# Kernel tuning notes

Measured on AMD Instinct MI355X. Metric: run time of the kernel, lower is better.

## Reference

```python
import jax, jax.numpy as jnp
import numpy as np
from functools import partial

V, E, H, F = 32000, 256, 512, 256  # vocab, embed_dim, hidden_dim, num_filters
FS = (3, 4, 5)

def setup_inputs() -> dict:
    key = jax.random.key(0)
    ks = jax.random.split(key, 24)
    s = 0.02
    d = {}
    d["src"] = jax.random.randint(ks[0], (32, 512), 0, V)
    d["trg"] = jax.random.randint(ks[1], (32, 64), 0, V)
    # embeddings with padding_idx=0 zeroed
    d["enc_emb"] = (jax.random.normal(ks[2], (V, E)) * s).at[0].set(0.0)
    d["dec_emb"] = (jax.random.normal(ks[3], (V, E)) * s).at[0].set(0.0)
    # conv1d weights (out_channels=F, in_channels=E, kernel)
    d["conv_w3"] = jax.random.normal(ks[4], (F, E, 3)) * s
    d["conv_b3"] = jnp.zeros((F,))
    d["conv_w4"] = jax.random.normal(ks[5], (F, E, 4)) * s
    d["conv_b4"] = jnp.zeros((F,))
    d["conv_w5"] = jax.random.normal(ks[6], (F, E, 5)) * s
    d["conv_b5"] = jnp.zeros((F,))
    d["fc1_w"] = jax.random.normal(ks[7], (H, 3 * F)) * s
    d["fc1_b"] = jnp.zeros((H,))
    d["fc2_w"] = jax.random.normal(ks[8], (H, H)) * s
    d["fc2_b"] = jnp.zeros((H,))
    # 2-layer LSTM: layer1 input E+H, layer2 input H; gates order i,f,g,o
    d["w_ih1"] = jax.random.normal(ks[9], (4 * H, E + H)) * s
    d["w_hh1"] = jax.random.normal(ks[10], (4 * H, H)) * s
    d["b_ih1"] = jnp.zeros((4 * H,))
    d["b_hh1"] = jnp.zeros((4 * H,))
    d["w_ih2"] = jax.random.normal(ks[11], (4 * H, H)) * s
    d["w_hh2"] = jax.random.normal(ks[12], (4 * H, H)) * s
    d["b_ih2"] = jnp.zeros((4 * H,))
    d["b_hh2"] = jnp.zeros((4 * H,))
    d["out_w"] = jax.random.normal(ks[13], (V, H)) * s
    d["out_b"] = jnp.zeros((V,))
    return d

def _lstm_cell(x, h, c, w_ih, w_hh, b_ih, b_hh):
    gates = x @ w_ih.T + b_ih + h @ w_hh.T + b_hh  # (B, 4H)
    i, f, g, o = jnp.split(gates, 4, axis=-1)
    c_new = jax.nn.sigmoid(f) * c + jax.nn.sigmoid(i) * jnp.tanh(g)
    h_new = jax.nn.sigmoid(o) * jnp.tanh(c_new)
    return h_new, c_new

def _encoder(src, enc_emb, convs, fc1_w, fc1_b, fc2_w, fc2_b):
    x = enc_emb[src]                    # (B, S, E)
    x = jnp.transpose(x, (0, 2, 1))     # (B, E, S)
    pooled = []
    for w, b in convs:
        y = jax.lax.conv_general_dilated(
            x, w, window_strides=(1,), padding='VALID',
            dimension_numbers=('NCH', 'OIH', 'NCH'))  # (B, F, S-k+1)
        pooled.append(jnp.max(jax.nn.relu(y + b[None, :, None]), axis=2))
    cat = jnp.concatenate(pooled, axis=1)              # (B, 3F)
    h = jax.nn.relu(cat @ fc1_w.T + fc1_b)             # (B, H)
    return h @ fc2_w.T + fc2_b                         # (B, H)

def reference(src, trg, enc_emb, conv_w3, conv_b3, conv_w4, conv_b4,
              conv_w5, conv_b5, fc1_w, fc1_b, fc2_w, fc2_b, dec_emb,
              w_ih1, w_hh1, b_ih1, b_hh1, w_ih2, w_hh2, b_ih2, b_hh2,
              out_w, out_b):
    B, T = trg.shape
    enc_out = _encoder(src, enc_emb,
                       [(conv_w3, conv_b3), (conv_w4, conv_b4), (conv_w5, conv_b5)],
                       fc1_w, fc1_b, fc2_w, fc2_b)  # (B, H)

    def step(carry, tok):
        h1, c1, h2, c2 = carry
        x = jnp.concatenate([dec_emb[tok], enc_out], axis=1)  # (B, E+H)
        h1, c1 = _lstm_cell(x, h1, c1, w_ih1, w_hh1, b_ih1, b_hh1)
        h2, c2 = _lstm_cell(h1, h2, c2, w_ih2, w_hh2, b_ih2, b_hh2)
        logits = h2 @ out_w.T + out_b                          # (B, V)
        return (h1, c1, h2, c2), logits

    z = jnp.zeros((B, H), dtype=enc_out.dtype)
    tokens = trg[:, :-1].T  # teacher forcing (ratio=1.0): (T-1, B)
    _, logits = jax.lax.scan(step, (z, z, z, z), tokens)       # (T-1, B, V)
    logits = jnp.transpose(logits, (1, 0, 2))                  # (B, T-1, V)
    # outputs[:, 0] is left as zeros, matching the torch loop starting at t=1
    return jnp.concatenate([jnp.zeros((B, 1, logits.shape[-1]), logits.dtype), logits], axis=1)
```

## Files before the change

kernel.cpp:

```cpp
#include <hip/hip_runtime.h>
#include <math.h>
#include <stdint.h>

#define B_    32
#define E_    256
#define F_    256
#define H_    512
#define V_    32000
#define G4    2048

typedef unsigned short u16;
typedef unsigned long long u64;
typedef __attribute__((ext_vector_type(8))) short bf16x8;
typedef __attribute__((ext_vector_type(4))) float f32x4;

__device__ __forceinline__ float fsig(float x) {
  return __builtin_amdgcn_rcpf(1.f + __expf(-x));
}
__device__ __forceinline__ float ftanh(float x) {
  return 1.f - 2.f * __builtin_amdgcn_rcpf(1.f + __expf(2.f * x));
}

__device__ __forceinline__ u16 f2bf(float f) {
  uint32_t u = __float_as_uint(f);
  uint32_t r = (u + 0x7FFFu + ((u >> 16) & 1u)) >> 16;
  return (u16)r;
}
__device__ __forceinline__ uint32_t pack2(float a, float b) {
  return (uint32_t)f2bf(a) | ((uint32_t)f2bf(b) << 16);
}

#define GLOAD16(gp, lp) __builtin_amdgcn_global_load_lds( \
    (const __attribute__((address_space(1))) uint32_t*)(const void*)(gp), \
    (__attribute__((address_space(3))) uint32_t*)(void*)(lp), 16, 0, 0)

#define ALOAD(P) __hip_atomic_load((P), __ATOMIC_RELAXED, __HIP_MEMORY_SCOPE_AGENT)
#define ASTORE(P, V) __hip_atomic_store((P), (V), __ATOMIC_RELAXED, __HIP_MEMORY_SCOPE_AGENT)

__global__ void prep_all(float* pooled, uint32_t* sent1, uint32_t* sent2,
                         uint32_t* cnt1, u16* h1d, u16* h2a,
                         const float* bi1, const float* bh1,
                         const float* bi2, const float* bh2,
                         float* bs1, float* bs2, float* out,
                         const float* s0, u16* d0, const float* s1, u16* d1,
                         const float* s2, u16* d2, const float* s3, u16* d3,
                         const float* s4, u16* d4,
                         const float* w3, u16* t3, const float* w4, u16* t4,
                         const float* w5, u16* t5) {
  int i = blockIdx.x * blockDim.x + threadIdx.x, st = gridDim.x * blockDim.x;
  for (int k = i; k < 2637824; k += st) {
    int j = k; const float* s; u16* d;
    if (j < 2048000) { s = s0; d = d0; }
    else if ((j -= 2048000) < 196608) { s = s1; d = d1; }
    else if ((j -= 196608) < 131072) { s = s2; d = d2; }
    else if ((j -= 131072) < 131072) { s = s3; d = d3; }
    else { j -= 131072; s = s4; d = d4; }
    const float4* sp = (const float4*)s + 2 * (size_t)j;
    float4 a = sp[0], b = sp[1];
    uint4 u;
    u.x = pack2(a.x, a.y); u.y = pack2(a.z, a.w);
    u.z = pack2(b.x, b.y); u.w = pack2(b.z, b.w);
    *((uint4*)d + j) = u;
  }
  for (int k = i; k < 786432; k += st) {
    int j = k; const float* w; u16* wt; int kw;
    if (j < 196608) { w = w3; wt = t3; kw = 3; }
    else if ((j -= 196608) < 262144) { w = w4; wt = t4; kw = 4; }
    else { j -= 262144; w = w5; wt = t5; kw = 5; }
    int f = j / (kw * 256);
    int r = j - f * (kw * 256);
    int jj = r >> 8, e = r & 255;
    wt[j] = f2bf(w[(f * 256 + e) * kw + jj]);
  }
  for (int k = i; k < 24576; k += st) pooled[k] = 0.f;
  for (int k = i; k < 131072; k += st) {
    uint32_t v = (k < 2048 && (k & 15) == 0) ? 1u : 0u;
    sent1[k] = v; sent2[k] = v;
  }
  for (int k = i; k < 256; k += st) cnt1[k] = 0u;
  uint4 z = {0u, 0u, 0u, 0u};
  for (int k = i; k < 2048; k += st) { ((uint4*)h1d)[k] = z; ((uint4*)h2a)[k] = z; }
  for (int k = i; k < G4; k += st) { bs1[k] = bi1[k] + bh1[k]; bs2[k] = bi2[k] + bh2[k]; }
  for (int k = i; k < B_ * V_; k += st) {
    int b = k / V_, v = k - b * V_;
    __builtin_nontemporal_store(0.f, &out[(size_t)b * 64 * V_ + v]);
  }
}

__global__ void gemm_small(const float* __restrict__ A, const float* __restrict__ W,
                           const float* __restrict__ bias, float* __restrict__ C,
                           int K, int N, int relu) {
  int nl = threadIdx.x & 7, b = threadIdx.x >> 3;
  int n = blockIdx.x * 8 + nl;
  const float* a = A + b * K;
  const float* w = W + (size_t)n * K;
  float acc = 0.f;
  for (int k = 0; k < K; k += 4) {
    float4 av = *reinterpret_cast<const float4*>(&a[k]);
    float4 wv = *reinterpret_cast<const float4*>(&w[k]);
    acc = fmaf(av.x, wv.x, acc); acc = fmaf(av.y, wv.y, acc);
    acc = fmaf(av.z, wv.z, acc); acc = fmaf(av.w, wv.w, acc);
  }
  acc += bias[n];
  if (relu) acc = fmaxf(acc, 0.f);
  C[b * N + n] = acc;
}

__global__ __launch_bounds__(256)
void conv_mfma(const u16* __restrict__ wt3, const u16* __restrict__ wt4,
               const u16* __restrict__ wt5,
               const float* __restrict__ cb3, const float* __restrict__ cb4,
               const float* __restrict__ cb5,
               float* __restrict__ pooled,
               const int* __restrict__ srcTok, const float* __restrict__ emb) {
  const int z = blockIdx.z;
  const u16* Bw = (z == 0) ? wt3 : (z == 1) ? wt4 : wt5;
  const float* bias = (z == 0) ? cb3 : (z == 1) ? cb4 : cb5;
  const int K = 768 + 256 * z, kw = 3 + z, poolOff = 256 * z;

  __shared__ char smem[32768];
  const int tid = threadIdx.x;
  const int wid = tid >> 6, lane = tid & 63;
  const int hi = lane >> 4, lo = lane & 15;
  const int wr = wid >> 1, wc = wid & 1;
  const int m0 = blockIdx.x * 128, n0 = blockIdx.y * 128;
  const int NT = K >> 5;
  const int srow = lane >> 2, sc = lane & 3;

  f32x4 acc[4][4];
#pragma unroll
  for (int i = 0; i < 4; ++i)
#pragma unroll
    for (int j = 0; j < 4; ++j) acc[i][j] = (f32x4){0.f, 0.f, 0.f, 0.f};

  for (int t = -1; t < NT; ++t) {
    int ts = t + 1;
    if (ts < NT) {
      char* base = smem + (ts & 1) * 16384;
      int k0 = ts << 5;
      {
        int j = k0 >> 8, e0 = k0 & 255;
        int row = tid >> 1;
        int m = m0 + row;
        int s = m & 511, b = m >> 9;
        int sj = s + j;
        int tok = (sj < 512) ? srcTok[b * 512 + sj] : -1;
#pragma unroll
        for (int q = 0; q < 2; ++q) {
          int cg = (tid & 1) * 2 + q;
          uint4 u;
          if (tok >= 0) {
            const float* ep = emb + (size_t)tok * 256 + e0 + cg * 8;
            float4 f0 = *(const float4*)(ep);
            float4 f1 = *(const float4*)(ep + 4);
            u.x = pack2(f0.x, f0.y); u.y = pack2(f0.z, f0.w);
            u.z = pack2(f1.x, f1.y); u.w = pack2(f1.z, f1.w);
          } else u = (uint4){0, 0, 0, 0};
          int c = cg ^ (row & 3);
          *(uint4*)(base + row * 64 + c * 16) = u;
        }
      }
#pragma unroll
      for (int q = 0; q < 2; ++q) {
        int row = (wid + q * 4) * 16 + srow;
        int gc = sc ^ (row & 3);
        const char* gp = (const char*)Bw + (((size_t)(n0 + row) * K + k0) << 1) + gc * 16;
        GLOAD16(gp, base + 8192 + (wid + q * 4) * 1024);
      }
    }
    if (t >= 0) {
      char* base = smem + (t & 1) * 16384;
      bf16x8 af[4], bfr[4];
#pragma unroll
      for (int mi = 0; mi < 4; ++mi) {
        int row = wr * 64 + mi * 16 + lo;
        af[mi] = *(const bf16x8*)(base + row * 64 + ((hi ^ (row & 3)) << 4));
      }
#pragma unroll
      for (int ni = 0; ni < 4; ++ni) {
        int row = wc * 64 + ni * 16 + lo;
        bfr[ni] = *(const bf16x8*)(base + 8192 + row * 64 + ((hi ^ (row & 3)) << 4));
      }
#pragma unroll
      for (int mi = 0; mi < 4; ++mi)
#pragma unroll
        for (int ni = 0; ni < 4; ++ni)
          acc[mi][ni] = __builtin_amdgcn_mfma_f32_16x16x32_bf16(af[mi], bfr[ni], acc[mi][ni], 0, 0, 0);
    }
    __syncthreads();
  }

  int b = m0 >> 9;
  int slim = 512 - kw;
#pragma unroll
  for (int ni = 0; ni < 4; ++ni) {
    int col = n0 + wc * 64 + ni * 16 + lo;
    float bv = bias[col];
    float mx = 0.f;
#pragma unroll
    for (int mi = 0; mi < 4; ++mi)
#pragma unroll
      for (int r = 0; r < 4; ++r) {
        int m = m0 + wr * 64 + mi * 16 + hi * 4 + r;
        int s = m & 511;
        float v = acc[mi][ni][r] + bv;
        if (s <= slim && v > mx) mx = v;
      }
    atomicMax((int*)&pooled[b * 768 + poolOff + col], __float_as_int(mx));
  }
}

__global__ __launch_bounds__(256, 1)
void lstm_fused(float* __restrict__ pre,
                const u16* __restrict__ whh1,
                const u16* __restrict__ wih2, const u16* __restrict__ whh2,
                const float* __restrict__ bs2,
                uint32_t* __restrict__ sent1, uint32_t* __restrict__ sent2,
                uint32_t* __restrict__ cnt1,
                u16* __restrict__ h1d, u16* __restrict__ h2a,
                const u16* __restrict__ outw_bf, const float* __restrict__ outb,
                float* __restrict__ out,
                const int* __restrict__ trg, const float* __restrict__ demb,
                const float* __restrict__ enco,
                const u16* __restrict__ wih1_bf, const float* __restrict__ bs1) {
  __shared__ char smem[74752];
  const int tid = threadIdx.x;
  const int wid = tid >> 6, lane = tid & 63, hi = lane >> 4, lo = lane & 15;
  const int hrow = tid >> 3, k8 = tid & 7;
  const int pb = hrow, pj0 = k8 * 2;

#define WAVE_DRAIN() asm volatile("s_waitcnt vmcnt(0)" ::: "memory")
#define POLL1(P) while (ALOAD(P) == 0u) __builtin_amdgcn_s_sleep(1);
#define POLL2(P, Q) for (;;) { uint32_t x_ = ALOAD(P), y_ = ALOAD(Q); \
                               if (x_ & y_) break; __builtin_amdgcn_s_sleep(1); }
#define POLL2S(P, Q) for (;;) { uint32_t x_ = ALOAD(P), y_ = ALOAD(Q); \
                                if (x_ & y_) break; __builtin_amdgcn_s_sleep(16); }

  if (blockIdx.x < 32) {
    const int bi = blockIdx.x;
    u16* hlds = (u16*)smem;
    float* glds = (float*)(smem + 33280);

    bf16x8 wreg[16];
    const u16* wp = whh1 + (((size_t)(wid * 512 + bi * 16 + lo)) << 9) + hi * 8;
#pragma unroll
    for (int ks = 0; ks < 16; ++ks) wreg[ks] = *(const bf16x8*)(wp + ks * 32);

    float creg0 = 0.f, creg1 = 0.f;

    for (int t = 0; t < 63; ++t) {
      if ((t & 3) == 0) {
        if (tid == 0)
          while (ALOAD(cnt1 + (t >> 2) * 16) < 16u) __builtin_amdgcn_s_sleep(8);
        __syncthreads();
      }
      const float* pr = pre + (((size_t)(t * 32 + pb)) << 11) + bi * 16 + pj0;
      float pi0 = pr[0], pf0 = pr[512], pg0 = pr[1024], po0 = pr[1536];
      float pi1 = pr[1], pf1 = pr[513], pg1 = pr[1025], po1 = pr[1537];

      const u64* hp = (const u64*)(h1d + ((size_t)t * 32 + hrow) * 512);
      f32x4 acc0 = (f32x4){0.f,0.f,0.f,0.f}, acc1 = (f32x4){0.f,0.f,0.f,0.f};

      POLL1(sent1 + (size_t)t * 2048 + lane * 16)
      {
        u64 v[8];
#pragma unroll
        for (int g = 0; g < 4; ++g) {
          int c = k8 + 8 * g;
          v[2*g]   = ALOAD(hp + 2 * c);
          v[2*g+1] = ALOAD(hp + 2 * c + 1);
        }
#pragma unroll
        for (int g = 0; g < 4; ++g) {
          int c = k8 + 8 * g;
          u64 w2[2] = { v[2*g], v[2*g+1] };
          *(uint4*)(hlds + hrow * 520 + c * 8) = *(const uint4*)w2;
        }
      }
      __syncthreads();
#pragma unroll
      for (int ks = 0; ks < 8; ++ks) {
        int cg = (ks * 4 + hi) * 8;
        bf16x8 a0 = *(const bf16x8*)(hlds + lo * 520 + cg);
        bf16x8 a1 = *(const bf16x8*)(hlds + (16 + lo) * 520 + cg);
        acc0 = __builtin_amdgcn_mfma_f32_16x16x32_bf16(a0, wreg[ks], acc0, 0, 0, 0);
        acc1 = __builtin_amdgcn_mfma_f32_16x16x32_bf16(a1, wreg[ks], acc1, 0, 0, 0);
      }
      POLL1(sent1 + (size_t)t * 2048 + (64 + lane) * 16)
      {
        u64 v[8];
#pragma unroll
        for (int g = 0; g < 4; ++g) {
          int c = 32 + k8 + 8 * g;
          v[2*g]   = ALOAD(hp + 2 * c);
          v[2*g+1] = ALOAD(hp + 2 * c + 1);
        }
#pragma unroll
        for (int g = 0; g < 4; ++g) {
          int c = 32 + k8 + 8 * g;
          u64 w2[2] = { v[2*g], v[2*g+1] };
          *(uint4*)(hlds + hrow * 520 + c * 8) = *(const uint4*)w2;
        }
      }
      __syncthreads();
#pragma unroll
      for (int ks = 8; ks < 16; ++ks) {
        int cg = (ks * 4 + hi) * 8;
        bf16x8 a0 = *(const bf16x8*)(hlds + lo * 520 + cg);
        bf16x8 a1 = *(const bf16x8*)(hlds + (16 + lo) * 520 + cg);
        acc0 = __builtin_amdgcn_mfma_f32_16x16x32_bf16(a0, wreg[ks], acc0, 0, 0, 0);
        acc1 = __builtin_amdgcn_mfma_f32_16x16x32_bf16(a1, wreg[ks], acc1, 0, 0, 0);
      }
#pragma unroll
      for (int r = 0; r < 4; ++r) {
        glds[wid * 544 + (hi * 4 + r) * 17 + lo] = acc0[r];
        glds[wid * 544 + (16 + hi * 4 + r) * 17 + lo] = acc1[r];
      }
      __syncthreads();

      float iv0 = glds[0*544 + pb*17 + pj0]   + pi0, fv0 = glds[1*544 + pb*17 + pj0]   + pf0;
      float gv0 = glds[2*544 + pb*17 + pj0]   + pg0, ov0 = glds[3*544 + pb*17 + pj0]   + po0;
      float iv1 = glds[0*544 + pb*17 + pj0+1] + pi1, fv1 = glds[1*544 + pb*17 + pj0+1] + pf1;
      float gv1 = glds[2*544 + pb*17 + pj0+1] + pg1, ov1 = glds[3*544 + pb*17 + pj0+1] + po1;
      float cn0 = fsig(fv0) * creg0 + fsig(iv0) * ftanh(gv0);
      float hn0 = fsig(ov0) * ftanh(cn0);
      float cn1 = fsig(fv1) * creg1 + fsig(iv1) * ftanh(gv1);
      float hn1 = fsig(ov1) * ftanh(cn1);
      creg0 = cn0; creg1 = cn1;
      ASTORE((uint32_t*)(h1d + ((size_t)(t + 1) * 32 + pb) * 512 + bi * 16 + pj0),
             pack2(hn0, hn1));
      WAVE_DRAIN();
      if (lane == 0)
        ASTORE(sent1 + (size_t)(t + 1) * 2048 + (bi * 4 + wid) * 16, 1u);
    }
  } else if (blockIdx.x < 64) {
    const int bi2 = blockIdx.x - 32;
    u16* alds = (u16*)smem;
    float* glds = (float*)(smem + 66048);

    bf16x8 wreg[32];
    {
      const u16* wa = wih2 + (((size_t)(wid * 512 + bi2 * 16 + lo)) << 9) + hi * 8;
      const u16* wb = whh2 + (((size_t)(wid * 512 + bi2 * 16 + lo)) << 9) + hi * 8;
#pragma unroll
      for (int ks = 0; ks < 16; ++ks) {
        wreg[ks]      = *(const bf16x8*)(wa + ks * 32);
        wreg[16 + ks] = *(const bf16x8*)(wb + ks * 32);
      }
    }
    float bsv0 = bs2[0 * 512 + bi2 * 16 + pj0], bsv0b = bs2[0 * 512 + bi2 * 16 + pj0 + 1];
    float bsv1 = bs2[1 * 512 + bi2 * 16 + pj0], bsv1b = bs2[1 * 512 + bi2 * 16 + pj0 + 1];
    float bsv2 = bs2[2 * 512 + bi2 * 16 + pj0], bsv2b = bs2[2 * 512 + bi2 * 16 + pj0 + 1];
    float bsv3 = bs2[3 * 512 + bi2 * 16 + pj0], bsv3b = bs2[3 * 512 + bi2 * 16 + pj0 + 1];

    float creg0 = 0.f, creg1 = 0.f;

    for (int t = 0; t < 63; ++t) {
      f32x4 acc0 = (f32x4){0.f,0.f,0.f,0.f}, acc1 = (f32x4){0.f,0.f,0.f,0.f};

      POLL2(sent1 + (size_t)(t + 1) * 2048 + lane * 16,
            sent1 + (size_t)(t + 1) * 2048 + (64 + lane) * 16)
      {
        const u64* hp1 = (const u64*)(h1d + ((size_t)(t + 1) * 32 + hrow) * 512);
        u64 v[16];
#pragma unroll
        for (int g = 0; g < 8; ++g) {
          int c = k8 + 8 * g;
          v[2*g]   = ALOAD(hp1 + 2 * c);
          v[2*g+1] = ALOAD(hp1 + 2 * c + 1);
        }
#pragma unroll
        for (int g = 0; g < 8; ++g) {
          int c = k8 + 8 * g;
          u64 w2[2] = { v[2*g], v[2*g+1] };
          *(uint4*)(alds + hrow * 1032 + c * 8) = *(const uint4*)w2;
        }
      }
      __syncthreads();
#pragma unroll
      for (int ks = 0; ks < 16; ++ks) {
        int cg = (ks * 4 + hi) * 8;
        bf16x8 a0 = *(const bf16x8*)(alds + lo * 1032 + cg);
        bf16x8 a1 = *(const bf16x8*)(alds + (16 + lo) * 1032 + cg);
        acc0 = __builtin_amdgcn_mfma_f32_16x16x32_bf16(a0, wreg[ks], acc0, 0, 0, 0);
        acc1 = __builtin_amdgcn_mfma_f32_16x16x32_bf16(a1, wreg[ks], acc1, 0, 0, 0);
      }
      POLL2(sent2 + (size_t)t * 2048 + lane * 16,
            sent2 + (size_t)t * 2048 + (64 + lane) * 16)
      {
        const u64* hp2 = (const u64*)(h2a + ((size_t)t * 32 + hrow) * 512);
        u64 v[16];
#pragma unroll
        for (int g = 0; g < 8; ++g) {
          int c = k8 + 8 * g;
          v[2*g]   = ALOAD(hp2 + 2 * c);
          v[2*g+1] = ALOAD(hp2 + 2 * c + 1);
        }
#pragma unroll
        for (int g = 0; g < 8; ++g) {
          int c = 64 + k8 + 8 * g;
          u64 w2[2] = { v[2*g], v[2*g+1] };
          *(uint4*)(alds + hrow * 1032 + c * 8) = *(const uint4*)w2;
        }
      }
      __syncthreads();
#pragma unroll
      for (int ks = 0; ks < 16; ++ks) {
        int cg = (64 + ks * 4 + hi) * 8;
        bf16x8 a0 = *(const bf16x8*)(alds + lo * 1032 + cg);
        bf16x8 a1 = *(const bf16x8*)(alds + (16 + lo) * 1032 + cg);
        acc0 = __builtin_amdgcn_mfma_f32_16x16x32_bf16(a0, wreg[16 + ks], acc0, 0, 0, 0);
        acc1 = __builtin_amdgcn_mfma_f32_16x16x32_bf16(a1, wreg[16 + ks], acc1, 0, 0, 0);
      }
#pragma unroll
      for (int r = 0; r < 4; ++r) {
        glds[wid * 544 + (hi * 4 + r) * 17 + lo] = acc0[r];
        glds[wid * 544 + (16 + hi * 4 + r) * 17 + lo] = acc1[r];
      }
      __syncthreads();

      float gi0 = glds[0*544 + pb*17 + pj0]   + bsv0,  gf0 = glds[1*544 + pb*17 + pj0]   + bsv1;
      float gg0 = glds[2*544 + pb*17 + pj0]   + bsv2,  go0 = glds[3*544 + pb*17 + pj0]   + bsv3;
      float gi1 = glds[0*544 + pb*17 + pj0+1] + bsv0b, gf1 = glds[1*544 + pb*17 + pj0+1] + bsv1b;
      float gg1 = glds[2*544 + pb*17 + pj0+1] + bsv2b, go1 = glds[3*544 + pb*17 + pj0+1] + bsv3b;
      float cn0 = fsig(gf0) * creg0 + fsig(gi0) * ftanh(gg0);
      float hn0 = fsig(go0) * ftanh(cn0);
      float cn1 = fsig(gf1) * creg1 + fsig(gi1) * ftanh(gg1);
      float hn1 = fsig(go1) * ftanh(cn1);
      creg0 = cn0; creg1 = cn1;
      ASTORE((uint32_t*)(h2a + ((size_t)(t + 1) * 32 + pb) * 512 + bi2 * 16 + pj0),
             pack2(hn0, hn1));
      WAVE_DRAIN();
      if (lane == 0)
        ASTORE(sent2 + (size_t)(t + 1) * 2048 + (bi2 * 4 + wid) * 16, 1u);
    }
  } else {
    const int bid2 = blockIdx.x - 64;
    const int wr = wid >> 1, wc = wid & 1;
    const int srow = lane >> 2, sc = lane & 3;

    for (int w = bid2; w < 256; w += 160) {
      int rt = w >> 4, ct = w & 15;
      const int m0 = rt * 128, n0 = ct * 128;
      f32x4 acc[4][4];
#pragma unroll
      for (int i = 0; i < 4; ++i)
#pragma unroll
        for (int j = 0; j < 4; ++j) acc[i][j] = (f32x4){0.f, 0.f, 0.f, 0.f};

      for (int t = -1; t < 24; ++t) {
        int ts = t + 1;
        if (ts < 24) {
          char* base = smem + (ts & 1) * 16384;
          int k0 = ts << 5;
          {
            int row = tid >> 1;
            int m = m0 + row;
            int tt = m >> 5, b = m & 31;
            int ok = (m < 2016);
            int tok = ok ? trg[b * 64 + tt] : 0;
#pragma unroll
            for (int q = 0; q < 2; ++q) {
              int cg = (tid & 1) * 2 + q;
              int k = k0 + cg * 8;
              uint4 u;
              if (ok) {
                const float* ep = (k < 256) ? (demb + (size_t)tok * 256 + k)
                                            : (enco + (size_t)b * 512 + (k - 256));
                float4 f0 = *(const float4*)(ep);
                float4 f1 = *(const float4*)(ep + 4);
                u.x = pack2(f0.x, f0.y); u.y = pack2(f0.z, f0.w);
                u.z = pack2(f1.x, f1.y); u.w = pack2(f1.z, f1.w);
              } else u = (uint4){0, 0, 0, 0};
              int c = cg ^ (row & 3);
              *(uint4*)(base + row * 64 + c * 16) = u;
            }
          }
#pragma unroll
          for (int q = 0; q < 2; ++q) {
            int row = (wid + q * 4) * 16 + srow;
            int gc = sc ^ (row & 3);
            const char* gp = (const char*)wih1_bf + (((size_t)(n0 + row) * 768 + k0) << 1) + gc * 16;
            GLOAD16(gp, base + 8192 + (wid + q * 4) * 1024);
          }
        }
        if (t >= 0) {
          char* base = smem + (t & 1) * 16384;
          bf16x8 af[4], bfr[4];
#pragma unroll
          for (int mi = 0; mi < 4; ++mi) {
            int row = wr * 64 + mi * 16 + lo;
            af[mi] = *(const bf16x8*)(base + row * 64 + ((hi ^ (row & 3)) << 4));
          }
#pragma unroll
          for (int ni = 0; ni < 4; ++ni) {
            int row = wc * 64 + ni * 16 + lo;
            bfr[ni] = *(const bf16x8*)(base + 8192 + row * 64 + ((hi ^ (row & 3)) << 4));
          }
#pragma unroll
          for (int mi = 0; mi < 4; ++mi)
#pragma unroll
            for (int ni = 0; ni < 4; ++ni)
              acc[mi][ni] = __builtin_amdgcn_mfma_f32_16x16x32_bf16(af[mi], bfr[ni], acc[mi][ni], 0, 0, 0);
        }
        __syncthreads();
      }
#pragma unroll
      for (int mi = 0; mi < 4; ++mi)
#pragma unroll
        for (int r = 0; r < 4; ++r) {
          int m = m0 + wr * 64 + mi * 16 + hi * 4 + r;
          if (m >= 2016) continue;
#pragma unroll
          for (int ni = 0; ni < 4; ++ni) {
            int col = n0 + wc * 64 + ni * 16 + lo;
            ASTORE((uint32_t*)(pre + (size_t)m * 2048 + col),
                   __float_as_uint(acc[mi][ni][r] + bs1[col]));
          }
        }
      WAVE_DRAIN();
      __syncthreads();
      if (tid == 0)
        __hip_atomic_fetch_add(cnt1 + rt * 16, 1u, __ATOMIC_RELAXED, __HIP_MEMORY_SCOPE_AGENT);
      __syncthreads();
    }

    const u16* A = h2a + 16384;

    for (int ct = bid2; ct < 250; ct += 160) {
      for (int rt = 0; rt < 16; ++rt) {
        int tf = rt * 4 + 4; if (tf > 63) tf = 63;
        if (wid == 0)
          POLL2S(sent2 + (size_t)tf * 2048 + lane * 16,
                 sent2 + (size_t)tf * 2048 + (64 + lane) * 16)
        __syncthreads();

        const int m0 = rt * 128, n0 = ct * 128;
        f32x4 acc[4][4];
#pragma unroll
        for (int i = 0; i < 4; ++i)
#pragma unroll
          for (int j = 0; j < 4; ++j) acc[i][j] = (f32x4){0.f, 0.f, 0.f, 0.f};

        for (int t = -1; t < 16; ++t) {
          int ts = t + 1;
          if (ts < 16) {
            char* base = smem + (ts & 1) * 16384;
            int k0 = ts << 5;
#pragma unroll
            for (int q = 0; q < 2; ++q) {
              int row = (wid + q * 4) * 16 + srow;
              int gc = sc ^ (row & 3);
              const char* gp = (const char*)A + (((size_t)(m0 + row) * 512 + k0) << 1) + gc * 16;
              GLOAD16(gp, base + (wid + q * 4) * 1024);
            }
#pragma unroll
            for (int q = 0; q < 2; ++q) {
              int row = (wid + q * 4) * 16 + srow;
              int gc = sc ^ (row & 3);
              const char* gp = (const char*)outw_bf + (((size_t)(n0 + row) * 512 + k0) << 1) + gc * 16;
              GLOAD16(gp, base + 8192 + (wid + q * 4) * 1024);
            }
          }
          if (t >= 0) {
            char* base = smem + (t & 1) * 16384;
            bf16x8 af[4], bfr[4];
#pragma unroll
            for (int mi = 0; mi < 4; ++mi) {
              int row = wr * 64 + mi * 16 + lo;
              af[mi] = *(const bf16x8*)(base + row * 64 + ((hi ^ (row & 3)) << 4));
            }
#pragma unroll
            for (int ni = 0; ni < 4; ++ni) {
              int row = wc * 64 + ni * 16 + lo;
              bfr[ni] = *(const bf16x8*)(base + 8192 + row * 64 + ((hi ^ (row & 3)) << 4));
            }
#pragma unroll
            for (int mi = 0; mi < 4; ++mi)
#pragma unroll
              for (int ni = 0; ni < 4; ++ni)
                acc[mi][ni] = __builtin_amdgcn_mfma_f32_16x16x32_bf16(af[mi], bfr[ni], acc[mi][ni], 0, 0, 0);
          }
          __syncthreads();
        }

#pragma unroll
        for (int mi = 0; mi < 4; ++mi)
#pragma unroll
          for (int r = 0; r < 4; ++r) {
            int m = m0 + wr * 64 + mi * 16 + hi * 4 + r;
            if (m >= 2016) continue;
            int t2 = m >> 5, b = m & 31;
            size_t rowbase = ((size_t)b * 64 + t2 + 1) * (size_t)V_;
#pragma unroll
            for (int ni = 0; ni < 4; ++ni) {
              int col = n0 + wc * 64 + ni * 16 + lo;
              __builtin_nontemporal_store(acc[mi][ni][r] + outb[col], &out[rowbase + col]);
            }
          }
      }
    }
  }
#undef POLL1
#undef POLL2
#undef POLL2S
#undef WAVE_DRAIN
}

extern "C" void kernel_launch(void* const* d_in, const int* in_sizes, int n_in,
                              void* d_out, int out_size, void* d_ws, size_t ws_size,
                              hipStream_t stream) {
  const int*   src  = (const int*)  d_in[0];
  const int*   trg  = (const int*)  d_in[1];
  const float* eemb = (const float*)d_in[2];
  const float* demb = (const float*)d_in[3];
  const float* cw3  = (const float*)d_in[4];
  const float* cb3  = (const float*)d_in[5];
  const float* cw4  = (const float*)d_in[6];
  const float* cb4  = (const float*)d_in[7];
  const float* cw5  = (const float*)d_in[8];
  const float* cb5  = (const float*)d_in[9];
  const float* fc1w = (const float*)d_in[10];
  const float* fc1b = (const float*)d_in[11];
  const float* fc2w = (const float*)d_in[12];
  const float* fc2b = (const float*)d_in[13];
  const float* wih1 = (const float*)d_in[14];
  const float* whh1 = (const float*)d_in[15];
  const float* bih1 = (const float*)d_in[16];
  const float* bhh1 = (const float*)d_in[17];
  const float* wih2 = (const float*)d_in[18];
  const float* whh2 = (const float*)d_in[19];
  const float* bih2 = (const float*)d_in[20];
  const float* bhh2 = (const float*)d_in[21];
  const float* outw = (const float*)d_in[22];
  const float* outb = (const float*)d_in[23];
  float* out = (float*)d_out;

  uint32_t* sent1 = (uint32_t*)d_ws;
  uint32_t* sent2 = sent1 + 131072;
  uint32_t* cnt1  = sent2 + 131072;
  u16* h1d      = (u16*)(cnt1 + 256);
  u16* h2a      = h1d + 1048576;
  float* pooled = (float*)(h2a + 1048576);
  float* ench   = pooled + 24576;
  float* enco   = ench + 16384;
  float* bs1    = enco + 16384;
  float* bs2    = bs1 + 2048;
  float* pre    = bs2 + 2048;
  u16* outw_bf  = (u16*)(pre + 4128768);
  u16* wih1_bf  = outw_bf + 16384000;
  u16* wih2_bf  = wih1_bf + 1572864;
  u16* whh1_bf  = wih2_bf + 1048576;
  u16* whh2_bf  = whh1_bf + 1048576;
  u16* wtj3     = whh2_bf + 1048576;
  u16* wtj4     = wtj3 + 196608;
  u16* wtj5     = wtj4 + 262144;

  prep_all<<<1024, 256, 0, stream>>>(pooled, sent1, sent2, cnt1, h1d, h2a,
                                     bih1, bhh1, bih2, bhh2, bs1, bs2, out,
                                     outw, outw_bf, wih1, wih1_bf, wih2, wih2_bf,
                                     whh1, whh1_bf, whh2, whh2_bf,
                                     cw3, wtj3, cw4, wtj4, cw5, wtj5);

  conv_mfma<<<dim3(128, 2, 3), 256, 0, stream>>>(wtj3, wtj4, wtj5, cb3, cb4, cb5,
                                                 pooled, src, eemb);
  gemm_small<<<64, 256, 0, stream>>>(pooled, fc1w, fc1b, ench, 768, 512, 1);
  gemm_small<<<64, 256, 0, stream>>>(ench, fc2w, fc2b, enco, 512, 512, 0);

  lstm_fused<<<224, 256, 0, stream>>>(pre, whh1_bf, wih2_bf, whh2_bf, bs2,
                                      sent1, sent2, cnt1, h1d, h2a,
                                      outw_bf, outb, out,
                                      trg, demb, enco, wih1_bf, bs1);
}
```

Baseline: 576.7 us.

## Fuse encoder conv, FC layers and weight casts into persistent LSTM kernel

Moves the conv+maxpool MFMA encoder, both FC layers, and the out_w bf16 conversion into the persistent lstm_fused kernel's worker blocks, coordinated by atomic counters. The LSTM recurrent weights are now converted from fp32 to bf16 directly into registers at kernel start instead of in a separate prep pass. The output GEMM loop is reordered by row-tile batches so earlier time steps can be processed first. This removes several kernel launches and serial dependencies so encoder work and weight casting can overlap with the LSTM recurrence, at the cost of spin-wait synchronisation and more complex inter-block ordering.

After: 635.1 us. 1.1x slower.

```diff
diff --git a/kernel.cpp b/kernel.cpp
--- a/kernel.cpp
+++ b/kernel.cpp
@@ -37,30 +37,22 @@
 #define ALOAD(P) __hip_atomic_load((P), __ATOMIC_RELAXED, __HIP_MEMORY_SCOPE_AGENT)
 #define ASTORE(P, V) __hip_atomic_store((P), (V), __ATOMIC_RELAXED, __HIP_MEMORY_SCOPE_AGENT)
 
-__global__ void prep_all(float* pooled, uint32_t* sent1, uint32_t* sent2,
-                         uint32_t* cnt1, u16* h1d, u16* h2a,
-                         const float* bi1, const float* bh1,
-                         const float* bi2, const float* bh2,
-                         float* bs1, float* bs2, float* out,
-                         const float* s0, u16* d0, const float* s1, u16* d1,
-                         const float* s2, u16* d2, const float* s3, u16* d3,
-                         const float* s4, u16* d4,
-                         const float* w3, u16* t3, const float* w4, u16* t4,
-                         const float* w5, u16* t5) {
+__global__ void prep_small(float* pooled, uint32_t* sent1, uint32_t* sent2,
+                           uint32_t* cnt1, uint32_t* cnts, u16* h1d, u16* h2a,
+                           const float* bi1, const float* bh1,
+                           const float* bi2, const float* bh2,
+                           float* bs1, float* bs2, float* out,
+                           const float* wih1, u16* wih1_bf,
+                           const float* w3, u16* t3, const float* w4, u16* t4,
+                           const float* w5, u16* t5) {
   int i = blockIdx.x * blockDim.x + threadIdx.x, st = gridDim.x * blockDim.x;
-  for (int k = i; k < 2637824; k += st) {
-    int j = k; const float* s; u16* d;
-    if (j < 2048000) { s = s0; d = d0; }
-    else if ((j -= 2048000) < 196608) { s = s1; d = d1; }
-    else if ((j -= 196608) < 131072) { s = s2; d = d2; }
-    else if ((j -= 131072) < 131072) { s = s3; d = d3; }
-    else { j -= 131072; s = s4; d = d4; }
-    const float4* sp = (const float4*)s + 2 * (size_t)j;
+  for (int j = i; j < 196608; j += st) {
+    const float4* sp = (const float4*)wih1 + 2 * (size_t)j;
     float4 a = sp[0], b = sp[1];
     uint4 u;
     u.x = pack2(a.x, a.y); u.y = pack2(a.z, a.w);
     u.z = pack2(b.x, b.y); u.w = pack2(b.z, b.w);
-    *((uint4*)d + j) = u;
+    *((uint4*)wih1_bf + j) = u;
   }
   for (int k = i; k < 786432; k += st) {
     int j = k; const float* w; u16* wt; int kw;
@@ -78,6 +70,7 @@
     sent1[k] = v; sent2[k] = v;
   }
   for (int k = i; k < 256; k += st) cnt1[k] = 0u;
+  for (int k = i; k < 64; k += st) cnts[k] = 0u;
   uint4 z = {0u, 0u, 0u, 0u};
   for (int k = i; k < 2048; k += st) { ((uint4*)h1d)[k] = z; ((uint4*)h2a)[k] = z; }
   for (int k = i; k < G4; k += st) { bs1[k] = bi1[k] + bh1[k]; bs2[k] = bi2[k] + bh2[k]; }
@@ -87,142 +80,27 @@
   }
 }
 
-__global__ void gemm_small(const float* __restrict__ A, const float* __restrict__ W,
-                           const float* __restrict__ bias, float* __restrict__ C,
-                           int K, int N, int relu) {
-  int nl = threadIdx.x & 7, b = threadIdx.x >> 3;
-  int n = blockIdx.x * 8 + nl;
-  const float* a = A + b * K;
-  const float* w = W + (size_t)n * K;
-  float acc = 0.f;
-  for (int k = 0; k < K; k += 4) {
-    float4 av = *reinterpret_cast<const float4*>(&a[k]);
-    float4 wv = *reinterpret_cast<const float4*>(&w[k]);
-    acc = fmaf(av.x, wv.x, acc); acc = fmaf(av.y, wv.y, acc);
-    acc = fmaf(av.z, wv.z, acc); acc = fmaf(av.w, wv.w, acc);
-  }
-  acc += bias[n];
-  if (relu) acc = fmaxf(acc, 0.f);
-  C[b * N + n] = acc;
-}
-
-__global__ __launch_bounds__(256)
-void conv_mfma(const u16* __restrict__ wt3, const u16* __restrict__ wt4,
-               const u16* __restrict__ wt5,
-               const float* __restrict__ cb3, const float* __restrict__ cb4,
-               const float* __restrict__ cb5,
-               float* __restrict__ pooled,
-               const int* __restrict__ srcTok, const float* __restrict__ emb) {
-  const int z = blockIdx.z;
-  const u16* Bw = (z == 0) ? wt3 : (z == 1) ? wt4 : wt5;
-  const float* bias = (z == 0) ? cb3 : (z == 1) ? cb4 : cb5;
-  const int K = 768 + 256 * z, kw = 3 + z, poolOff = 256 * z;
-
-  __shared__ char smem[32768];
-  const int tid = threadIdx.x;
-  const int wid = tid >> 6, lane = tid & 63;
-  const int hi = lane >> 4, lo = lane & 15;
-  const int wr = wid >> 1, wc = wid & 1;
-  const int m0 = blockIdx.x * 128, n0 = blockIdx.y * 128;
-  const int NT = K >> 5;
-  const int srow = lane >> 2, sc = lane & 3;
-
-  f32x4 acc[4][4];
-#pragma unroll
-  for (int i = 0; i < 4; ++i)
-#pragma unroll
-    for (int j = 0; j < 4; ++j) acc[i][j] = (f32x4){0.f, 0.f, 0.f, 0.f};
-
-  for (int t = -1; t < NT; ++t) {
-    int ts = t + 1;
-    if (ts < NT) {
-      char* base = smem + (ts & 1) * 16384;
-      int k0 = ts << 5;
-      {
-        int j = k0 >> 8, e0 = k0 & 255;
-        int row = tid >> 1;
-        int m = m0 + row;
-        int s = m & 511, b = m >> 9;
-        int sj = s + j;
-        int tok = (sj < 512) ? srcTok[b * 512 + sj] : -1;
-#pragma unroll
-        for (int q = 0; q < 2; ++q) {
-          int cg = (tid & 1) * 2 + q;
-          uint4 u;
-          if (tok >= 0) {
-            const float* ep = emb + (size_t)tok * 256 + e0 + cg * 8;
-            float4 f0 = *(const float4*)(ep);
-            float4 f1 = *(const float4*)(ep + 4);
-            u.x = pack2(f0.x, f0.y); u.y = pack2(f0.z, f0.w);
-            u.z = pack2(f1.x, f1.y); u.w = pack2(f1.z, f1.w);
-          } else u = (uint4){0, 0, 0, 0};
-          int c = cg ^ (row & 3);
-          *(uint4*)(base + row * 64 + c * 16) = u;
-        }
-      }
-#pragma unroll
-      for (int q = 0; q < 2; ++q) {
-        int row = (wid + q * 4) * 16 + srow;
-        int gc = sc ^ (row & 3);
-        const char* gp = (const char*)Bw + (((size_t)(n0 + row) * K + k0) << 1) + gc * 16;
-        GLOAD16(gp, base + 8192 + (wid + q * 4) * 1024);
-      }
-    }
-    if (t >= 0) {
-      char* base = smem + (t & 1) * 16384;
-      bf16x8 af[4], bfr[4];
-#pragma unroll
-      for (int mi = 0; mi < 4; ++mi) {
-        int row = wr * 64 + mi * 16 + lo;
-        af[mi] = *(const bf16x8*)(base + row * 64 + ((hi ^ (row & 3)) << 4));
-      }
-#pragma unroll
-      for (int ni = 0; ni < 4; ++ni) {
-        int row = wc * 64 + ni * 16 + lo;
-        bfr[ni] = *(const bf16x8*)(base + 8192 + row * 64 + ((hi ^ (row & 3)) << 4));
-      }
-#pragma unroll
-      for (int mi = 0; mi < 4; ++mi)
-#pragma unroll
-        for (int ni = 0; ni < 4; ++ni)
-          acc[mi][ni] = __builtin_amdgcn_mfma_f32_16x16x32_bf16(af[mi], bfr[ni], acc[mi][ni], 0, 0, 0);
-    }
-    __syncthreads();
-  }
-
-  int b = m0 >> 9;
-  int slim = 512 - kw;
-#pragma unroll
-  for (int ni = 0; ni < 4; ++ni) {
-    int col = n0 + wc * 64 + ni * 16 + lo;
-    float bv = bias[col];
-    float mx = 0.f;
-#pragma unroll
-    for (int mi = 0; mi < 4; ++mi)
-#pragma unroll
-      for (int r = 0; r < 4; ++r) {
-        int m = m0 + wr * 64 + mi * 16 + hi * 4 + r;
-        int s = m & 511;
-        float v = acc[mi][ni][r] + bv;
-        if (s <= slim && v > mx) mx = v;
-      }
-    atomicMax((int*)&pooled[b * 768 + poolOff + col], __float_as_int(mx));
-  }
-}
-
 __global__ __launch_bounds__(256, 1)
 void lstm_fused(float* __restrict__ pre,
-                const u16* __restrict__ whh1,
-                const u16* __restrict__ wih2, const u16* __restrict__ whh2,
+                const float* __restrict__ whh1f,
+                const float* __restrict__ wih2f, const float* __restrict__ whh2f,
                 const float* __restrict__ bs2,
                 uint32_t* __restrict__ sent1, uint32_t* __restrict__ sent2,
-                uint32_t* __restrict__ cnt1,
+                uint32_t* __restrict__ cnt1, uint32_t* __restrict__ cnts,
                 u16* __restrict__ h1d, u16* __restrict__ h2a,
-                const u16* __restrict__ outw_bf, const float* __restrict__ outb,
-                float* __restrict__ out,
+                const float* __restrict__ outwf, u16* __restrict__ outw_bf,
+                const float* __restrict__ outb, float* __restrict__ out,
                 const int* __restrict__ trg, const float* __restrict__ demb,
-                const float* __restrict__ enco,
-                const u16* __restrict__ wih1_bf, const float* __restrict__ bs1) {
+                float* __restrict__ enco,
+                const u16* __restrict__ wih1_bf, const float* __restrict__ bs1,
+                const int* __restrict__ src, const float* __restrict__ eemb,
+                const u16* __restrict__ wtj3, const u16* __restrict__ wtj4,
+                const u16* __restrict__ wtj5,
+                const float* __restrict__ cb3, const float* __restrict__ cb4,
+                const float* __restrict__ cb5,
+                const float* __restrict__ fc1w, const float* __restrict__ fc1b,
+                const float* __restrict__ fc2w, const float* __restrict__ fc2b,
+                float* __restrict__ pooled, float* __restrict__ ench) {
   __shared__ char smem[74752];
   const int tid = threadIdx.x;
   const int wid = tid >> 6, lane = tid & 63, hi = lane >> 4, lo = lane & 15;
@@ -235,6 +113,8 @@
                                if (x_ & y_) break; __builtin_amdgcn_s_sleep(1); }
 #define POLL2S(P, Q) for (;;) { uint32_t x_ = ALOAD(P), y_ = ALOAD(Q); \
                                 if (x_ & y_) break; __builtin_amdgcn_s_sleep(16); }
+#define WAITCNT(P, TGT) { if (tid == 0) while (ALOAD(P) < (uint32_t)(TGT)) \
+                            __builtin_amdgcn_s_sleep(8); __syncthreads(); }
 
   if (blockIdx.x < 32) {
     const int bi = blockIdx.x;
@@ -242,18 +122,23 @@
     float* glds = (float*)(smem + 33280);
 
     bf16x8 wreg[16];
-    const u16* wp = whh1 + (((size_t)(wid * 512 + bi * 16 + lo)) << 9) + hi * 8;
-#pragma unroll
-    for (int ks = 0; ks < 16; ++ks) wreg[ks] = *(const bf16x8*)(wp + ks * 32);
+    {
+      const float* wp = whh1f + (((size_t)(wid * 512 + bi * 16 + lo)) << 9) + hi * 8;
+#pragma unroll
+      for (int ks = 0; ks < 16; ++ks) {
+        float4 f0 = *(const float4*)(wp + ks * 32);
+        float4 f1 = *(const float4*)(wp + ks * 32 + 4);
+        uint4 uu;
+        uu.x = pack2(f0.x, f0.y); uu.y = pack2(f0.z, f0.w);
+        uu.z = pack2(f1.x, f1.y); uu.w = pack2(f1.z, f1.w);
+        wreg[ks] = *(bf16x8*)&uu;
+      }
+    }
 
     float creg0 = 0.f, creg1 = 0.f;
 
     for (int t = 0; t < 63; ++t) {
-      if ((t & 3) == 0) {
-        if (tid == 0)
-          while (ALOAD(cnt1 + (t >> 2) * 16) < 16u) __builtin_amdgcn_s_sleep(8);
-        __syncthreads();
-      }
+      if ((t & 3) == 0) WAITCNT(cnt1 + (t >> 2) * 16, 16)
       const float* pr = pre + (((size_t)(t * 32 + pb)) << 11) + bi * 16 + pj0;
       float pi0 = pr[0], pf0 = pr[512], pg0 = pr[1024], po0 = pr[1536];
       float pi1 = pr[1], pf1 = pr[513], pg1 = pr[1025], po1 = pr[1537];
@@ -340,12 +225,21 @@
 
     bf16x8 wreg[32];
     {
-      const u16* wa = wih2 + (((size_t)(wid * 512 + bi2 * 16 + lo)) << 9) + hi * 8;
-      const u16* wb = whh2 + (((size_t)(wid * 512 + bi2 * 16 + lo)) << 9) + hi * 8;
+      const float* wa = wih2f + (((size_t)(wid * 512 + bi2 * 16 + lo)) << 9) + hi * 8;
+      const float* wb = whh2f + (((size_t)(wid * 512 + bi2 * 16 + lo)) << 9) + hi * 8;
 #pragma unroll
       for (int ks = 0; ks < 16; ++ks) {
-        wreg[ks]      = *(const bf16x8*)(wa + ks * 32);
-        wreg[16 + ks] = *(const bf16x8*)(wb + ks * 32);
+        float4 f0 = *(const float4*)(wa + ks * 32);
+        float4 f1 = *(const float4*)(wa + ks * 32 + 4);
+        uint4 uu;
+        uu.x = pack2(f0.x, f0.y); uu.y = pack2(f0.z, f0.w);
+        uu.z = pack2(f1.x, f1.y); uu.w = pack2(f1.z, f1.w);
+        wreg[ks] = *(bf16x8*)&uu;
+        f0 = *(const float4*)(wb + ks * 32);
+        f1 = *(const float4*)(wb + ks * 32 + 4);
+        uu.x = pack2(f0.x, f0.y); uu.y = pack2(f0.z, f0.w);
+        uu.z = pack2(f1.x, f1.y); uu.w = pack2(f1.z, f1.w);
+        wreg[16 + ks] = *(bf16x8*)&uu;
       }
     }
     float bsv0 = bs2[0 * 512 + bi2 * 16 + pj0], bsv0b = bs2[0 * 512 + bi2 * 16 + pj0 + 1];
@@ -439,6 +333,160 @@
     const int wr = wid >> 1, wc = wid & 1;
     const int srow = lane >> 2, sc = lane & 3;
 
+    for (int w = bid2; w < 768; w += 160) {
+      int z = w >> 8, r2 = w & 255, mt = r2 >> 1, nt = r2 & 1;
+      const u16* Bw = (z == 0) ? wtj3 : (z == 1) ? wtj4 : wtj5;
+      const float* bias = (z == 0) ? cb3 : (z == 1) ? cb4 : cb5;
+      const int K = 768 + 256 * z, kw = 3 + z, poolOff = 256 * z;
+      const int m0 = mt * 128, n0 = nt * 128;
+      const int NT = K >> 5;
+
+      f32x4 acc[4][4];
+#pragma unroll
+      for (int i = 0; i < 4; ++i)
+#pragma unroll
+        for (int j = 0; j < 4; ++j) acc[i][j] = (f32x4){0.f, 0.f, 0.f, 0.f};
+
+      for (int t = -1; t < NT; ++t) {
+        int ts = t + 1;
+        if (ts < NT) {
+          char* base = smem + (ts & 1) * 16384;
+          int k0 = ts << 5;
+          {
+            int j = k0 >> 8, e0 = k0 & 255;
+            int row = tid >> 1;
+            int m = m0 + row;
+            int s = m & 511, b = m >> 9;
+            int sj = s + j;
+            int tok = (sj < 512) ? src[b * 512 + sj] : -1;
+#pragma unroll
+            for (int q = 0; q < 2; ++q) {
+              int cg = (tid & 1) * 2 + q;
+              uint4 u;
+              if (tok >= 0) {
+                const float* ep = eemb + (size_t)tok * 256 + e0 + cg * 8;
+                float4 f0 = *(const float4*)(ep);
+                float4 f1 = *(const float4*)(ep + 4);
+                u.x = pack2(f0.x, f0.y); u.y = pack2(f0.z, f0.w);
+                u.z = pack2(f1.x, f1.y); u.w = pack2(f1.z, f1.w);
+              } else u = (uint4){0, 0, 0, 0};
+              int c = cg ^ (row & 3);
+              *(uint4*)(base + row * 64 + c * 16) = u;
+            }
+          }
+#pragma unroll
+          for (int q = 0; q < 2; ++q) {
+            int row = (wid + q * 4) * 16 + srow;
+            int gc = sc ^ (row & 3);
+            const char* gp = (const char*)Bw + (((size_t)(n0 + row) * K + k0) << 1) + gc * 16;
+            GLOAD16(gp, base + 8192 + (wid + q * 4) * 1024);
+          }
+        }
+        if (t >= 0) {
+          char* base = smem + (t & 1) * 16384;
+          bf16x8 af[4], bfr[4];
+#pragma unroll
+          for (int mi = 0; mi < 4; ++mi) {
+            int row = wr * 64 + mi * 16 + lo;
+            af[mi] = *(const bf16x8*)(base + row * 64 + ((hi ^ (row & 3)) << 4));
+          }
+#pragma unroll
+          for (int ni = 0; ni < 4; ++ni) {
+            int row = wc * 64 + ni * 16 + lo;
+            bfr[ni] = *(const bf16x8*)(base + 8192 + row * 64 + ((hi ^ (row & 3)) << 4));
+          }
+#pragma unroll
+          for (int mi = 0; mi < 4; ++mi)
+#pragma unroll
+            for (int ni = 0; ni < 4; ++ni)
+              acc[mi][ni] = __builtin_amdgcn_mfma_f32_16x16x32_bf16(af[mi], bfr[ni], acc[mi][ni], 0, 0, 0);
+        }
+        __syncthreads();
+      }
+
+      int b = m0 >> 9;
+      int slim = 512 - kw;
+#pragma unroll
+      for (int ni = 0; ni < 4; ++ni) {
+        int col = n0 + wc * 64 + ni * 16 + lo;
+        float bv = bias[col];
+        float mx = 0.f;
+#pragma unroll
+        for (int mi = 0; mi < 4; ++mi)
+#pragma unroll
+          for (int r = 0; r < 4; ++r) {
+            int m = m0 + wr * 64 + mi * 16 + hi * 4 + r;
+            int s = m & 511;
+            float v = acc[mi][ni][r] + bv;
+            if (s <= slim && v > mx) mx = v;
+          }
+        atomicMax((int*)&pooled[b * 768 + poolOff + col], __float_as_int(mx));
+      }
+      __syncthreads();
+    }
+    WAVE_DRAIN();
+    __syncthreads();
+    if (tid == 0)
+      __hip_atomic_fetch_add(cnts + 0, 1u, __ATOMIC_RELAXED, __HIP_MEMORY_SCOPE_AGENT);
+
+    if (bid2 < 64) {
+      WAITCNT(cnts + 0, 160)
+      {
+        int nl = tid & 7, b = tid >> 3;
+        int n = bid2 * 8 + nl;
+        const u64* ap = (const u64*)(pooled + b * 768);
+        const float* ww = fc1w + (size_t)n * 768;
+        float acc = 0.f;
+        for (int k = 0; k < 768; k += 2) {
+          u64 v = ALOAD(ap + (k >> 1));
+          float2 wv = *(const float2*)(ww + k);
+          acc = fmaf(__uint_as_float((uint32_t)v), wv.x,
+                fmaf(__uint_as_float((uint32_t)(v >> 32)), wv.y, acc));
+        }
+        acc += fc1b[n];
+        acc = fmaxf(acc, 0.f);
+        ASTORE((uint32_t*)(ench + b * 512 + n), __float_as_uint(acc));
+      }
+      WAVE_DRAIN();
+      __syncthreads();
+      if (tid == 0)
+        __hip_atomic_fetch_add(cnts + 16, 1u, __ATOMIC_RELAXED, __HIP_MEMORY_SCOPE_AGENT);
+      WAITCNT(cnts + 16, 64)
+      {
+        int nl = tid & 7, b = tid >> 3;
+        int n = bid2 * 8 + nl;
+        const u64* ap = (const u64*)(ench + b * 512);
+        const float* ww = fc2w + (size_t)n * 512;
+        float acc = 0.f;
+        for (int k = 0; k < 512; k += 2) {
+          u64 v = ALOAD(ap + (k >> 1));
+          float2 wv = *(const float2*)(ww + k);
+          acc = fmaf(__uint_as_float((uint32_t)v), wv.x,
+                fmaf(__uint_as_float((uint32_t)(v >> 32)), wv.y, acc));
+        }
+        acc += fc2b[n];
+        ASTORE((uint32_t*)(enco + b * 512 + n), __float_as_uint(acc));
+      }
+      WAVE_DRAIN();
+      __syncthreads();
+      if (tid == 0)
+        __hip_atomic_fetch_add(cnts + 32, 1u, __ATOMIC_RELAXED, __HIP_MEMORY_SCOPE_AGENT);
+    } else {
+      for (int j = (bid2 - 64) * 256 + tid; j < 2048000; j += 96 * 256) {
+        const float4* sp = (const float4*)outwf + 2 * (size_t)j;
+        float4 a = sp[0], b = sp[1];
+        uint4 u;
+        u.x = pack2(a.x, a.y); u.y = pack2(a.z, a.w);
+        u.z = pack2(b.x, b.y); u.w = pack2(b.z, b.w);
+        *((uint4*)outw_bf + j) = u;
+      }
+      WAVE_DRAIN();
+      __syncthreads();
+      if (tid == 0)
+        __hip_atomic_fetch_add(cnts + 48, 1u, __ATOMIC_RELAXED, __HIP_MEMORY_SCOPE_AGENT);
+    }
+
+    WAITCNT(cnts + 32, 64)
     for (int w = bid2; w < 256; w += 160) {
       int rt = w >> 4, ct = w & 15;
       const int m0 = rt * 128, n0 = ct * 128;
@@ -463,15 +511,23 @@
             for (int q = 0; q < 2; ++q) {
               int cg = (tid & 1) * 2 + q;
               int k = k0 + cg * 8;
-              uint4 u;
+              uint4 u = {0, 0, 0, 0};
               if (ok) {
-                const float* ep = (k < 256) ? (demb + (size_t)tok * 256 + k)
-                                            : (enco + (size_t)b * 512 + (k - 256));
-                float4 f0 = *(const float4*)(ep);
-                float4 f1 = *(const float4*)(ep + 4);
-                u.x = pack2(f0.x, f0.y); u.y = pack2(f0.z, f0.w);
-                u.z = pack2(f1.x, f1.y); u.w = pack2(f1.z, f1.w);
-              } else u = (uint4){0, 0, 0, 0};
+                if (k < 256) {
+                  const float* ep = demb + (size_t)tok * 256 + k;
+                  float4 f0 = *(const float4*)(ep);
+                  float4 f1 = *(const float4*)(ep + 4);
+                  u.x = pack2(f0.x, f0.y); u.y = pack2(f0.z, f0.w);
+                  u.z = pack2(f1.x, f1.y); u.w = pack2(f1.z, f1.w);
+                } else {
+                  const u64* e2 = (const u64*)(enco + (size_t)b * 512 + (k - 256));
+                  u64 v0 = ALOAD(e2), v1 = ALOAD(e2 + 1), v2 = ALOAD(e2 + 2), v3 = ALOAD(e2 + 3);
+                  u.x = pack2(__uint_as_float((uint32_t)v0), __uint_as_float((uint32_t)(v0 >> 32)));
+                  u.y = pack2(__uint_as_float((uint32_t)v1), __uint_as_float((uint32_t)(v1 >> 32)));
+                  u.z = pack2(__uint_as_float((uint32_t)v2), __uint_as_float((uint32_t)(v2 >> 32)));
+                  u.w = pack2(__uint_as_float((uint32_t)v3), __uint_as_float((uint32_t)(v3 >> 32)));
+                }
+              }
               int c = cg ^ (row & 3);
               *(uint4*)(base + row * 64 + c * 16) = u;
             }
@@ -525,10 +581,12 @@
       __syncthreads();
     }
 
+    WAITCNT(cnts + 48, 96)
     const u16* A = h2a + 16384;
 
-    for (int ct = bid2; ct < 250; ct += 160) {
-      for (int rt = 0; rt < 16; ++rt) {
+    for (int rtb = 0; rtb < 4; ++rtb) {
+      for (int w = bid2; w < 1000; w += 160) {
+        int rt = rtb * 4 + w / 250, ct = w - (w / 250) * 250;
         int tf = rt * 4 + 4; if (tf > 63) tf = 63;
         if (wid == 0)
           POLL2S(sent2 + (size_t)tf * 2048 + lane * 16,
@@ -604,6 +662,7 @@
 #undef POLL1
 #undef POLL2
 #undef POLL2S
+#undef WAITCNT
 #undef WAVE_DRAIN
 }
 
@@ -639,7 +698,8 @@
   uint32_t* sent1 = (uint32_t*)d_ws;
   uint32_t* sent2 = sent1 + 131072;
   uint32_t* cnt1  = sent2 + 131072;
-  u16* h1d      = (u16*)(cnt1 + 256);
+  uint32_t* cnts  = cnt1 + 256;
+  u16* h1d      = (u16*)(cnts + 64);
   u16* h2a      = h1d + 1048576;
   float* pooled = (float*)(h2a + 1048576);
   float* ench   = pooled + 24576;
@@ -649,26 +709,20 @@
   float* pre    = bs2 + 2048;
   u16* outw_bf  = (u16*)(pre + 4128768);
   u16* wih1_bf  = outw_bf + 16384000;
-  u16* wih2_bf  = wih1_bf + 1572864;
-  u16* whh1_bf  = wih2_bf + 1048576;
-  u16* whh2_bf  = whh1_bf + 1048576;
-  u16* wtj3     = whh2_bf + 1048576;
+  u16* wtj3     = wih1_bf + 1572864;
   u16* wtj4     = wtj3 + 196608;
   u16* wtj5     = wtj4 + 262144;
 
-  prep_all<<<1024, 256, 0, stream>>>(pooled, sent1, sent2, cnt1, h1d, h2a,
-                                     bih1, bhh1, bih2, bhh2, bs1, bs2, out,
-                                     outw, outw_bf, wih1, wih1_bf, wih2, wih2_bf,
-                                     whh1, whh1_bf, whh2, whh2_bf,
-                                     cw3, wtj3, cw4, wtj4, cw5, wtj5);
-
-  conv_mfma<<<dim3(128, 2, 3), 256, 0, stream>>>(wtj3, wtj4, wtj5, cb3, cb4, cb5,
-                                                 pooled, src, eemb);
-  gemm_small<<<64, 256, 0, stream>>>(pooled, fc1w, fc1b, ench, 768, 512, 1);
-  gemm_small<<<64, 256, 0, stream>>>(ench, fc2w, fc2b, enco, 512, 512, 0);
-
-  lstm_fused<<<224, 256, 0, stream>>>(pre, whh1_bf, wih2_bf, whh2_bf, bs2,
-                                      sent1, sent2, cnt1, h1d, h2a,
-                                      outw_bf, outb, out,
-                                      trg, demb, enco, wih1_bf, bs1);
+  prep_small<<<512, 256, 0, stream>>>(pooled, sent1, sent2, cnt1, cnts, h1d, h2a,
+                                      bih1, bhh1, bih2, bhh2, bs1, bs2, out,
+                                      wih1, wih1_bf,
+                                      cw3, wtj3, cw4, wtj4, cw5, wtj5);
+
+  lstm_fused<<<224, 256, 0, stream>>>(pre, whh1, wih2, whh2, bs2,
+                                      sent1, sent2, cnt1, cnts, h1d, h2a,
+                                      outw, outw_bf, outb, out,
+                                      trg, demb, enco, wih1_bf, bs1,
+                                      src, eemb, wtj3, wtj4, wtj5,
+                                      cb3, cb4, cb5,
+                                      fc1w, fc1b, fc2w, fc2b, pooled, ench);
 }
```
